# Optimization experiments

Hardware: AMD Instinct MI355X
Metric: run time of the kernel (lower is better)

## Reference

```python
import jax, jax.numpy as jnp
import numpy as np

B, N, DIM = 4, 2048, 1024
HEAD = 16
INTER = 1024
HD = INTER // HEAD  # 64
SCALE = INTER ** (-0.5)


def setup_inputs() -> dict:
    key = jax.random.key(0)
    k1, k2, k3 = jax.random.split(key, 3)
    features = jax.random.normal(k1, (B, N, DIM), dtype=jnp.float32)
    W_qkv = jax.random.normal(k2, (DIM, 3 * INTER), dtype=jnp.float32) * (DIM ** -0.5)
    W_out = jax.random.normal(k3, (INTER, DIM), dtype=jnp.float32) * (INTER ** -0.5)
    return {"features": features, "W_qkv": W_qkv, "W_out": W_out}


def reference(features, W_qkv, W_out):
    # fc_qkv: [b, n, 3*inter], chunk into q, k, v
    qkv = jnp.einsum('bnd,de->bne', features, W_qkv)
    q, k, v = jnp.split(qkv, 3, axis=-1)
    # b n (h d) -> b n h d
    q = q.reshape(B, N, HEAD, HD)
    k = k.reshape(B, N, HEAD, HD)
    v = v.reshape(B, N, HEAD, HD)
    # scores: b h i j  (scale = inter_dim ** -0.5, as in source)
    alpha = jnp.einsum('bihd,bjhd->bhij', q, k) * SCALE
    att = jax.nn.softmax(alpha, axis=-1)
    out = jnp.einsum('bhij,bjhd->bihd', att, v)
    out = out.reshape(B, N, INTER)
    # fc_out (dropout_ratio=0.0 -> identity)
    return jnp.einsum('bni,id->bnd', out, W_out)
```

## Files before the change

### kernel.cpp

```cpp
#include <hip/hip_runtime.h>
#include <stdint.h>

#define BB 4
#define SEQ 2048
#define DMODEL 1024
#define NHEAD 16
#define HDIM 64
#define INTER 1024
#define QSCALE 0.045084220027780106f

#if __has_builtin(__builtin_amdgcn_exp2f)
#define EXP2F(x) __builtin_amdgcn_exp2f(x)
#else
#define EXP2F(x) exp2f(x)
#endif

typedef unsigned short u16;
typedef __attribute__((ext_vector_type(4))) unsigned short u16x4;
typedef __attribute__((ext_vector_type(4))) short s16x4;
typedef __attribute__((ext_vector_type(8))) short s16x8;
typedef __attribute__((ext_vector_type(4))) float f32x4;
typedef __attribute__((ext_vector_type(16))) float f32x16;
typedef __attribute__((ext_vector_type(4))) unsigned int u32x4;

__device__ __forceinline__ u16 f2bf(float f) {
  unsigned int u = __float_as_uint(f);
  u += 0x7FFFu + ((u >> 16) & 1u);
  return (u16)(u >> 16);
}

#if __has_builtin(__builtin_amdgcn_cvt_pk_bf16_f32)
typedef __attribute__((ext_vector_type(2))) __bf16 bf16x2_t;
__device__ __forceinline__ unsigned int pk2bf(float a, float b) {
  bf16x2_t r = __builtin_amdgcn_cvt_pk_bf16_f32(a, b);
  return *reinterpret_cast<unsigned int*>(&r);
}
#else
__device__ __forceinline__ unsigned int pk2bf(float a, float b) {
  return (unsigned int)f2bf(a) | ((unsigned int)f2bf(b) << 16);
}
#endif

__device__ __forceinline__ void async16(const u16* g, u16* l) {
  __builtin_amdgcn_global_load_lds((__attribute__((address_space(1))) void*)(void*)(g),
                                   (__attribute__((address_space(3))) void*)(l),
                                   16, 0, 0);
}

__device__ __forceinline__ void make_pb(const unsigned int* cc, int half,
                                        s16x8& pb0, s16x8& pb1) {
#if __has_builtin(__builtin_amdgcn_permlane32_swap)
  (void)half;
  auto r02 = __builtin_amdgcn_permlane32_swap(cc[0], cc[2], false, false);
  auto r13 = __builtin_amdgcn_permlane32_swap(cc[1], cc[3], false, false);
  auto r46 = __builtin_amdgcn_permlane32_swap(cc[4], cc[6], false, false);
  auto r57 = __builtin_amdgcn_permlane32_swap(cc[5], cc[7], false, false);
  u32x4 w0 = {(unsigned)r02[0], (unsigned)r13[0], (unsigned)r02[1], (unsigned)r13[1]};
  u32x4 w1 = {(unsigned)r46[0], (unsigned)r57[0], (unsigned)r46[1], (unsigned)r57[1]};
#else
  unsigned x0 = __shfl_xor((int)cc[0], 32, 64), x1 = __shfl_xor((int)cc[1], 32, 64);
  unsigned x2 = __shfl_xor((int)cc[2], 32, 64), x3 = __shfl_xor((int)cc[3], 32, 64);
  unsigned x4 = __shfl_xor((int)cc[4], 32, 64), x5 = __shfl_xor((int)cc[5], 32, 64);
  unsigned x6 = __shfl_xor((int)cc[6], 32, 64), x7 = __shfl_xor((int)cc[7], 32, 64);
  u32x4 w0 = {half ? x2 : cc[0], half ? x3 : cc[1],
              half ? cc[2] : x0, half ? cc[3] : x1};
  u32x4 w1 = {half ? x6 : cc[4], half ? x7 : cc[5],
              half ? cc[6] : x4, half ? cc[7] : x5};
#endif
  pb0 = *reinterpret_cast<s16x8*>(&w0);
  pb1 = *reinterpret_cast<s16x8*>(&w1);
}

__global__ __launch_bounds__(256) void prep(
    const float* __restrict__ f, const float* __restrict__ wqkv,
    const float* __restrict__ wout, u16* __restrict__ Xb,
    u16* __restrict__ WqkvT, u16* __restrict__ WoutT) {
  __shared__ float tile[32][33];
  const int bid = blockIdx.x, tid = threadIdx.x;
  if (bid < 8192) {
    int i = (bid * 256 + tid) * 4;
    f32x4 v = *reinterpret_cast<const f32x4*>(f + i);
    uint2 o;
    o.x = pk2bf(v[0], v[1]);
    o.y = pk2bf(v[2], v[3]);
    *reinterpret_cast<uint2*>(Xb + i) = o;
  } else {
    const float* src; u16* dst; int rows, cols, bx, by;
    if (bid < 8192 + 3072) {
      int t = bid - 8192;
      src = wqkv; dst = WqkvT; rows = DMODEL; cols = 3 * INTER;
      bx = t % 96; by = t / 96;
    } else {
      int t = bid - 11264;
      src = wout; dst = WoutT; rows = INTER; cols = DMODEL;
      bx = t & 31; by = t >> 5;
    }
    int c0 = bx * 32, r0 = by * 32, tx = tid & 31, ty = tid >> 5;
    #pragma unroll
    for (int i = ty; i < 32; i += 8) tile[i][tx] = src[(size_t)(r0 + i) * cols + c0 + tx];
    __syncthreads();
    #pragma unroll
    for (int i = ty; i < 32; i += 8)
      dst[(size_t)(c0 + i) * rows + r0 + tx] = f2bf(tile[tx][i]);
  }
}

#define GCOMP(ABUF, BBUF)                                                         \
  {                                                                               \
    s16x8 af[4], bf[4];                                                           \
    _Pragma("unroll")                                                             \
    for (int t = 0; t < 4; t++) {                                                 \
      af[t] = *reinterpret_cast<const s16x8*>(&ABUF[(wr + t * 16 + r) * 32 + q8]); \
      bf[t] = *reinterpret_cast<const s16x8*>(&BBUF[(wc + t * 16 + r) * 32 + q8]); \
    }                                                                             \
    _Pragma("unroll")                                                             \
    for (int i = 0; i < 4; i++)                                                   \
      _Pragma("unroll")                                                           \
      for (int j = 0; j < 4; j++)                                                 \
        acc[i][j] = __builtin_amdgcn_mfma_f32_16x16x32_bf16(af[i], bf[j], acc[i][j], 0, 0, 0); \
  }

template <int MODE>
__global__ __launch_bounds__(256, 2) void gemm_bt(
    const u16* __restrict__ A, const u16* __restrict__ BT,
    float* __restrict__ Cf, u16* __restrict__ Qb, u16* __restrict__ Kp,
    u16* __restrict__ Vp, int K, int ldc) {
  __shared__ u16 As[2][128 * 32];
  __shared__ u16 Bs[2][128 * 32];
  const int tid = threadIdx.x;
  const int wave = tid >> 6, lane = tid & 63;
  const int row0 = blockIdx.y * 128, col0 = blockIdx.x * 128;
  const int wr = (wave >> 1) * 64, wc = (wave & 1) * 64;
  const int r = lane & 15, q8 = (lane >> 4) * 8;

  f32x4 acc[4][4] = {};

  const int sRow = lane >> 2, sK = (lane & 3) * 8;
  const u16* Ag0 = A + (size_t)(row0 + wave * 32 + sRow) * K + sK;
  const u16* Ag1 = Ag0 + (size_t)16 * K;
  const u16* Bg0 = BT + (size_t)(col0 + wave * 32 + sRow) * K + sK;
  const u16* Bg1 = Bg0 + (size_t)16 * K;
  u16* Al0a = &As[0][wave * 1024]; u16* Al1a = Al0a + 512;
  u16* Bl0a = &Bs[0][wave * 1024]; u16* Bl1a = Bl0a + 512;
  u16* Al0b = &As[1][wave * 1024]; u16* Al1b = Al0b + 512;
  u16* Bl0b = &Bs[1][wave * 1024]; u16* Bl1b = Bl0b + 512;

  async16(Ag0, Al0a);
  async16(Ag1, Al1a);
  async16(Bg0, Bl0a);
  async16(Bg1, Bl1a);
  __syncthreads();

  for (int k0 = 0; k0 < K; k0 += 64) {
    if (k0 + 32 < K) {
      async16(Ag0 + k0 + 32, Al0b);
      async16(Ag1 + k0 + 32, Al1b);
      async16(Bg0 + k0 + 32, Bl0b);
      async16(Bg1 + k0 + 32, Bl1b);
    }
    GCOMP(As[0], Bs[0])
    __syncthreads();
    if (k0 + 64 < K) {
      async16(Ag0 + k0 + 64, Al0a);
      async16(Ag1 + k0 + 64, Al1a);
      async16(Bg0 + k0 + 64, Bl0a);
      async16(Bg1 + k0 + 64, Bl1a);
    }
    GCOMP(As[1], Bs[1])
    __syncthreads();
  }

  const int quad = lane >> 4;
  #pragma unroll
  for (int i = 0; i < 4; i++) {
    const int n = row0 + wr + i * 16 + quad * 4;
    const int b = n >> 11, nn = n & (SEQ - 1);
    #pragma unroll
    for (int j = 0; j < 4; j++) {
      const int gc = col0 + wc + j * 16 + r;
      if (MODE == 1) {
        #pragma unroll
        for (int reg = 0; reg < 4; reg++)
          Cf[(size_t)(n + reg) * ldc + gc] = acc[i][j][reg];
      } else if (gc < INTER) {
        size_t base = (size_t)n * INTER + gc;
        #pragma unroll
        for (int reg = 0; reg < 4; reg++)
          Qb[base + (size_t)reg * INTER] = f2bf(acc[i][j][reg] * QSCALE);
      } else if (gc < 2 * INTER) {
        int dim = gc - INTER, h = dim >> 6, d = dim & 63;
        int bh = b * NHEAD + h;
        size_t base = (((size_t)(bh * 64 + (nn >> 5)) * 4 + (d >> 4)) * 64 +
                       ((((d >> 3) & 1) << 5) | (nn & 31))) * 8 + (d & 7);
        #pragma unroll
        for (int reg = 0; reg < 4; reg++)
          Kp[base + reg * 8] = f2bf(acc[i][j][reg]);
      } else {
        int dim = gc - 2 * INTER, h = dim >> 6, d = dim & 63;
        int bh = b * NHEAD + h;
        size_t base = ((((size_t)(bh * 64 + (nn >> 5)) * 2 + ((nn >> 4) & 1)) * 2 +
                        (d >> 5)) * 64 +
                       ((((nn >> 3) & 1) << 5) | (d & 31))) * 8 + (nn & 7);
        uint2 pk;
        pk.x = pk2bf(acc[i][j][0], acc[i][j][1]);
        pk.y = pk2bf(acc[i][j][2], acc[i][j][3]);
        *reinterpret_cast<uint2*>(Vp + base) = pk;
      }
    }
  }
}

#define PSTEP(JCUR, SCUR, SNXT, KNXT, KPF)                                        \
  {                                                                               \
    s16x8 vf[4];                                                                  \
    _Pragma("unroll")                                                             \
    for (int c = 0; c < 4; c++)                                                   \
      vf[c] = *reinterpret_cast<const s16x8*>(vpb + (JCUR) * 2048 + c * 512);     \
    const int jpf = ((JCUR) + 2) & 63;                                            \
    _Pragma("unroll")                                                             \
    for (int c = 0; c < 4; c++)                                                   \
      KPF[c] = *reinterpret_cast<const s16x8*>(kpb + jpf * 2048 + c * 512);       \
    SNXT = (f32x16){};                                                            \
    __builtin_amdgcn_s_setprio(1);                                                \
    _Pragma("unroll")                                                             \
    for (int c = 0; c < 4; c++)                                                   \
      SNXT = __builtin_amdgcn_mfma_f32_32x32x16_bf16(KNXT[c], qf[c], SNXT, 0, 0, 0); \
    __builtin_amdgcn_s_setprio(0);                                                \
    unsigned int cc[8];                                                           \
    _Pragma("unroll")                                                             \
    for (int q = 0; q < 4; q++) {                                                 \
      float p0 = EXP2F(SCUR[q * 4 + 0]), p1 = EXP2F(SCUR[q * 4 + 1]);             \
      float p2 = EXP2F(SCUR[q * 4 + 2]), p3 = EXP2F(SCUR[q * 4 + 3]);             \
      ls += (p0 + p1) + (p2 + p3);                                                \
      cc[q * 2 + 0] = pk2bf(p0, p1);                                              \
      cc[q * 2 + 1] = pk2bf(p2, p3);                                              \
    }                                                                             \
    s16x8 pb0, pb1;                                                               \
    make_pb(cc, half, pb0, pb1);                                                  \
    __builtin_amdgcn_s_setprio(1);                                                \
    ot0 = __builtin_amdgcn_mfma_f32_32x32x16_bf16(vf[0], pb0, ot0, 0, 0, 0);      \
    ot1 = __builtin_amdgcn_mfma_f32_32x32x16_bf16(vf[1], pb0, ot1, 0, 0, 0);      \
    ot0 = __builtin_amdgcn_mfma_f32_32x32x16_bf16(vf[2], pb1, ot0, 0, 0, 0);      \
    ot1 = __builtin_amdgcn_mfma_f32_32x32x16_bf16(vf[3], pb1, ot1, 0, 0, 0);      \
    __builtin_amdgcn_s_setprio(0);                                                \
  }

__global__ __launch_bounds__(64, 3) void attn_kernel(
    const u16* __restrict__ Qb, const u16* __restrict__ Kp,
    const u16* __restrict__ Vp, u16* __restrict__ AO) {
  const int lane = threadIdx.x;
  const int l31 = lane & 31, half = lane >> 5;
  const int bh = blockIdx.x, b = bh >> 4, h = bh & 15;
  const int i0 = blockIdx.y * 32;

  const u16* qbase = Qb + (size_t)(b * SEQ + i0 + l31) * INTER + h * HDIM + half * 8;
  s16x8 qf[4];
  #pragma unroll
  for (int c = 0; c < 4; c++) qf[c] = *reinterpret_cast<const s16x8*>(qbase + c * 16);

  const u16* kpb = Kp + (size_t)bh * (64 * 4 * 512) + lane * 8;
  const u16* vpb = Vp + (size_t)bh * (64 * 4 * 512) + lane * 8;

  f32x16 ot0 = {}, ot1 = {};
  float ls = 0.f;

  s16x8 kX[4], kY[4];
  #pragma unroll
  for (int c = 0; c < 4; c++)
    kX[c] = *reinterpret_cast<const s16x8*>(kpb + 0 * 2048 + c * 512);
  f32x16 stA = {}, stB;
  #pragma unroll
  for (int c = 0; c < 4; c++)
    stA = __builtin_amdgcn_mfma_f32_32x32x16_bf16(kX[c], qf[c], stA, 0, 0, 0);
  #pragma unroll
  for (int c = 0; c < 4; c++)
    kY[c] = *reinterpret_cast<const s16x8*>(kpb + 1 * 2048 + c * 512);

  for (int jb = 0; jb < 64; jb += 2) {
    PSTEP(jb,     stA, stB, kY, kX)
    PSTEP(jb + 1, stB, stA, kX, kY)
  }

  ls += __shfl_xor(ls, 32, 64);
  float rinv = 1.0f / ls;

  u16* orow = AO + (size_t)(b * SEQ + i0 + l31) * INTER + h * HDIM;
  #pragma unroll
  for (int dt = 0; dt < 2; dt++) {
    const f32x16& o = dt ? ot1 : ot0;
    #pragma unroll
    for (int q = 0; q < 4; q++) {
      uint2 pk;
      pk.x = pk2bf(o[q * 4 + 0] * rinv, o[q * 4 + 1] * rinv);
      pk.y = pk2bf(o[q * 4 + 2] * rinv, o[q * 4 + 3] * rinv);
      *reinterpret_cast<uint2*>(orow + dt * 32 + q * 8 + half * 4) = pk;
    }
  }
}

extern "C" void kernel_launch(void* const* d_in, const int* in_sizes, int n_in,
                              void* d_out, int out_size, void* d_ws, size_t ws_size,
                              hipStream_t stream) {
  const float* features = (const float*)d_in[0];
  const float* W_qkv    = (const float*)d_in[1];
  const float* W_out    = (const float*)d_in[2];
  float* out = (float*)d_out;
  char* w = (char*)d_ws;
  u16* Xb    = (u16*)(w);
  u16* WqkvT = (u16*)(w + 16777216);
  u16* WoutT = (u16*)(w + 23068672);
  u16* Qb    = (u16*)(w + 25165824);
  u16* Kp    = (u16*)(w + 41943040);
  u16* Vp    = (u16*)(w + 58720256);
  u16* AO    = (u16*)(w + 75497472);

  prep<<<dim3(12288), dim3(256), 0, stream>>>(features, W_qkv, W_out, Xb, WqkvT, WoutT);
  gemm_bt<0><<<dim3(24, 64), dim3(256), 0, stream>>>(Xb, WqkvT, nullptr, Qb, Kp, Vp,
                                                     DMODEL, 0);
  attn_kernel<<<dim3(64, 64), dim3(64), 0, stream>>>(Qb, Kp, Vp, AO);
  gemm_bt<1><<<dim3(8, 64), dim3(256), 0, stream>>>(AO, WoutT, out, nullptr, nullptr,
                                                    nullptr, INTER, DMODEL);
}
```

Before: 274.7 us.

## Replace QKV projection GEMM with 256x256-tile 8-wave pipelined kernel

Result: slower. 303.0 us (+10.3%).

```diff
diff --git a/kernel.cpp b/kernel.cpp
--- a/kernel.cpp
+++ b/kernel.cpp
@@ -105,84 +105,116 @@
   }
 }
 
-#define GCOMP(ABUF, BBUF)                                                         \
-  {                                                                               \
-    s16x8 af[4], bf[4];                                                           \
-    _Pragma("unroll")                                                             \
-    for (int t = 0; t < 4; t++) {                                                 \
-      af[t] = *reinterpret_cast<const s16x8*>(&ABUF[(wr + t * 16 + r) * 32 + q8]); \
-      bf[t] = *reinterpret_cast<const s16x8*>(&BBUF[(wc + t * 16 + r) * 32 + q8]); \
-    }                                                                             \
-    _Pragma("unroll")                                                             \
-    for (int i = 0; i < 4; i++)                                                   \
-      _Pragma("unroll")                                                           \
-      for (int j = 0; j < 4; j++)                                                 \
-        acc[i][j] = __builtin_amdgcn_mfma_f32_16x16x32_bf16(af[i], bf[j], acc[i][j], 0, 0, 0); \
-  }
-
-template <int MODE>
-__global__ __launch_bounds__(256, 2) void gemm_bt(
+__global__ __launch_bounds__(512, 2) void gemm8p(
     const u16* __restrict__ A, const u16* __restrict__ BT,
-    float* __restrict__ Cf, u16* __restrict__ Qb, u16* __restrict__ Kp,
-    u16* __restrict__ Vp, int K, int ldc) {
-  __shared__ u16 As[2][128 * 32];
-  __shared__ u16 Bs[2][128 * 32];
+    u16* __restrict__ Qb, u16* __restrict__ Kp, u16* __restrict__ Vp) {
+  __shared__ __align__(16) u16 As[2][256 * 64];
+  __shared__ __align__(16) u16 Bs[2][256 * 64];
   const int tid = threadIdx.x;
   const int wave = tid >> 6, lane = tid & 63;
-  const int row0 = blockIdx.y * 128, col0 = blockIdx.x * 128;
-  const int wr = (wave >> 1) * 64, wc = (wave & 1) * 64;
+  const int wm = wave >> 2, wn = wave & 3;
   const int r = lane & 15, q8 = (lane >> 4) * 8;
-
-  f32x4 acc[4][4] = {};
-
-  const int sRow = lane >> 2, sK = (lane & 3) * 8;
-  const u16* Ag0 = A + (size_t)(row0 + wave * 32 + sRow) * K + sK;
-  const u16* Ag1 = Ag0 + (size_t)16 * K;
-  const u16* Bg0 = BT + (size_t)(col0 + wave * 32 + sRow) * K + sK;
-  const u16* Bg1 = Bg0 + (size_t)16 * K;
-  u16* Al0a = &As[0][wave * 1024]; u16* Al1a = Al0a + 512;
-  u16* Bl0a = &Bs[0][wave * 1024]; u16* Bl1a = Bl0a + 512;
-  u16* Al0b = &As[1][wave * 1024]; u16* Al1b = Al0b + 512;
-  u16* Bl0b = &Bs[1][wave * 1024]; u16* Bl1b = Bl0b + 512;
-
-  async16(Ag0, Al0a);
-  async16(Ag1, Al1a);
-  async16(Bg0, Bl0a);
-  async16(Bg1, Bl1a);
-  __syncthreads();
-
-  for (int k0 = 0; k0 < K; k0 += 64) {
-    if (k0 + 32 < K) {
-      async16(Ag0 + k0 + 32, Al0b);
-      async16(Ag1 + k0 + 32, Al1b);
-      async16(Bg0 + k0 + 32, Bl0b);
-      async16(Bg1 + k0 + 32, Bl1b);
-    }
-    GCOMP(As[0], Bs[0])
-    __syncthreads();
-    if (k0 + 64 < K) {
-      async16(Ag0 + k0 + 64, Al0a);
-      async16(Ag1 + k0 + 64, Al1a);
-      async16(Bg0 + k0 + 64, Bl0a);
-      async16(Bg1 + k0 + 64, Bl1a);
-    }
-    GCOMP(As[1], Bs[1])
-    __syncthreads();
+  const int row0 = blockIdx.y * 256, col0 = blockIdx.x * 256;
+
+  const u16* Ag = A + (size_t)(row0 + (tid >> 3)) * 1024 + ((tid & 7) << 3);
+  const u16* Bg = BT + (size_t)(col0 + (tid >> 3)) * 1024 + ((tid & 7) << 3);
+  const int ldsSlot = tid * 8;
+
+  const int aBase = (wm * 128 + r) * 64 + q8;
+  const int bBase = (wn * 64 + r) * 64 + q8;
+
+  f32x4 acc[8][4] = {};
+
+  #pragma unroll
+  for (int i = 0; i < 4; i++) async16(Ag + i * 65536, &As[0][ldsSlot + i * 4096]);
+  #pragma unroll
+  for (int i = 0; i < 4; i++) async16(Bg + i * 65536, &Bs[0][ldsSlot + i * 4096]);
+  asm volatile("s_waitcnt vmcnt(0)" ::: "memory");
+  __builtin_amdgcn_s_barrier();
+
+  for (int kt = 0; kt < 16; kt++) {
+    const int cur = kt & 1;
+    const u16* Ac = &As[0][0] + cur * (256 * 64);
+    const u16* Bc = &Bs[0][0] + cur * (256 * 64);
+    u16* An = &As[0][0] + (1 - cur) * (256 * 64);
+    u16* Bn = &Bs[0][0] + (1 - cur) * (256 * 64);
+    const int kB = (kt + 1) * 64;
+
+    s16x8 af[4], bf[4];
+
+    #pragma unroll
+    for (int nf = 0; nf < 4; nf++)
+      bf[nf] = *reinterpret_cast<const s16x8*>(&Bc[bBase + nf * 1024]);
+    #pragma unroll
+    for (int mf = 0; mf < 4; mf++)
+      af[mf] = *reinterpret_cast<const s16x8*>(&Ac[aBase + mf * 1024]);
+    #pragma unroll
+    for (int i = 0; i < 4; i++) async16(Ag + kB + i * 65536, &An[ldsSlot + i * 4096]);
+    __builtin_amdgcn_s_barrier();
+    __builtin_amdgcn_s_setprio(1);
+    #pragma unroll
+    for (int mf = 0; mf < 4; mf++)
+      #pragma unroll
+      for (int nf = 0; nf < 4; nf++)
+        acc[mf][nf] = __builtin_amdgcn_mfma_f32_16x16x32_bf16(af[mf], bf[nf], acc[mf][nf], 0, 0, 0);
+    __builtin_amdgcn_s_setprio(0);
+    __builtin_amdgcn_s_barrier();
+
+    #pragma unroll
+    for (int mf = 0; mf < 4; mf++)
+      af[mf] = *reinterpret_cast<const s16x8*>(&Ac[aBase + (mf + 4) * 1024]);
+    #pragma unroll
+    for (int i = 0; i < 4; i++) async16(Bg + kB + i * 65536, &Bn[ldsSlot + i * 4096]);
+    __builtin_amdgcn_s_barrier();
+    __builtin_amdgcn_s_setprio(1);
+    #pragma unroll
+    for (int mf = 0; mf < 4; mf++)
+      #pragma unroll
+      for (int nf = 0; nf < 4; nf++)
+        acc[mf + 4][nf] = __builtin_amdgcn_mfma_f32_16x16x32_bf16(af[mf], bf[nf], acc[mf + 4][nf], 0, 0, 0);
+    __builtin_amdgcn_s_setprio(0);
+    __builtin_amdgcn_s_barrier();
+
+    #pragma unroll
+    for (int nf = 0; nf < 4; nf++)
+      bf[nf] = *reinterpret_cast<const s16x8*>(&Bc[bBase + nf * 1024 + 32]);
+    #pragma unroll
+    for (int mf = 0; mf < 4; mf++)
+      af[mf] = *reinterpret_cast<const s16x8*>(&Ac[aBase + mf * 1024 + 32]);
+    __builtin_amdgcn_s_barrier();
+    __builtin_amdgcn_s_setprio(1);
+    #pragma unroll
+    for (int mf = 0; mf < 4; mf++)
+      #pragma unroll
+      for (int nf = 0; nf < 4; nf++)
+        acc[mf][nf] = __builtin_amdgcn_mfma_f32_16x16x32_bf16(af[mf], bf[nf], acc[mf][nf], 0, 0, 0);
+    __builtin_amdgcn_s_setprio(0);
+    __builtin_amdgcn_s_barrier();
+
+    #pragma unroll
+    for (int mf = 0; mf < 4; mf++)
+      af[mf] = *reinterpret_cast<const s16x8*>(&Ac[aBase + (mf + 4) * 1024 + 32]);
+    __builtin_amdgcn_s_barrier();
+    __builtin_amdgcn_s_setprio(1);
+    #pragma unroll
+    for (int mf = 0; mf < 4; mf++)
+      #pragma unroll
+      for (int nf = 0; nf < 4; nf++)
+        acc[mf + 4][nf] = __builtin_amdgcn_mfma_f32_16x16x32_bf16(af[mf], bf[nf], acc[mf + 4][nf], 0, 0, 0);
+    __builtin_amdgcn_s_setprio(0);
+    asm volatile("s_waitcnt vmcnt(0)" ::: "memory");
+    __builtin_amdgcn_s_barrier();
   }
 
   const int quad = lane >> 4;
   #pragma unroll
-  for (int i = 0; i < 4; i++) {
-    const int n = row0 + wr + i * 16 + quad * 4;
+  for (int i = 0; i < 8; i++) {
+    const int n = row0 + wm * 128 + i * 16 + quad * 4;
     const int b = n >> 11, nn = n & (SEQ - 1);
     #pragma unroll
     for (int j = 0; j < 4; j++) {
-      const int gc = col0 + wc + j * 16 + r;
-      if (MODE == 1) {
-        #pragma unroll
-        for (int reg = 0; reg < 4; reg++)
-          Cf[(size_t)(n + reg) * ldc + gc] = acc[i][j][reg];
-      } else if (gc < INTER) {
+      const int gc = col0 + wn * 64 + j * 16 + r;
+      if (gc < INTER) {
         size_t base = (size_t)n * INTER + gc;
         #pragma unroll
         for (int reg = 0; reg < 4; reg++)
@@ -210,6 +242,83 @@
   }
 }
 
+#define GCOMP(ABUF, BBUF)                                                         \
+  {                                                                               \
+    s16x8 af[4], bf[4];                                                           \
+    _Pragma("unroll")                                                             \
+    for (int t = 0; t < 4; t++) {                                                 \
+      af[t] = *reinterpret_cast<const s16x8*>(&ABUF[(wr + t * 16 + r) * 32 + q8]); \
+      bf[t] = *reinterpret_cast<const s16x8*>(&BBUF[(wc + t * 16 + r) * 32 + q8]); \
+    }                                                                             \
+    _Pragma("unroll")                                                             \
+    for (int i = 0; i < 4; i++)                                                   \
+      _Pragma("unroll")                                                           \
+      for (int j = 0; j < 4; j++)                                                 \
+        acc[i][j] = __builtin_amdgcn_mfma_f32_16x16x32_bf16(af[i], bf[j], acc[i][j], 0, 0, 0); \
+  }
+
+__global__ __launch_bounds__(256, 2) void gemm_out(
+    const u16* __restrict__ A, const u16* __restrict__ BT,
+    float* __restrict__ Cf, int K, int ldc) {
+  __shared__ u16 As[2][128 * 32];
+  __shared__ u16 Bs[2][128 * 32];
+  const int tid = threadIdx.x;
+  const int wave = tid >> 6, lane = tid & 63;
+  const int row0 = blockIdx.y * 128, col0 = blockIdx.x * 128;
+  const int wr = (wave >> 1) * 64, wc = (wave & 1) * 64;
+  const int r = lane & 15, q8 = (lane >> 4) * 8;
+
+  f32x4 acc[4][4] = {};
+
+  const int sRow = lane >> 2, sK = (lane & 3) * 8;
+  const u16* Ag0 = A + (size_t)(row0 + wave * 32 + sRow) * K + sK;
+  const u16* Ag1 = Ag0 + (size_t)16 * K;
+  const u16* Bg0 = BT + (size_t)(col0 + wave * 32 + sRow) * K + sK;
+  const u16* Bg1 = Bg0 + (size_t)16 * K;
+  u16* Al0a = &As[0][wave * 1024]; u16* Al1a = Al0a + 512;
+  u16* Bl0a = &Bs[0][wave * 1024]; u16* Bl1a = Bl0a + 512;
+  u16* Al0b = &As[1][wave * 1024]; u16* Al1b = Al0b + 512;
+  u16* Bl0b = &Bs[1][wave * 1024]; u16* Bl1b = Bl0b + 512;
+
+  async16(Ag0, Al0a);
+  async16(Ag1, Al1a);
+  async16(Bg0, Bl0a);
+  async16(Bg1, Bl1a);
+  __syncthreads();
+
+  for (int k0 = 0; k0 < K; k0 += 64) {
+    if (k0 + 32 < K) {
+      async16(Ag0 + k0 + 32, Al0b);
+      async16(Ag1 + k0 + 32, Al1b);
+      async16(Bg0 + k0 + 32, Bl0b);
+      async16(Bg1 + k0 + 32, Bl1b);
+    }
+    GCOMP(As[0], Bs[0])
+    __syncthreads();
+    if (k0 + 64 < K) {
+      async16(Ag0 + k0 + 64, Al0a);
+      async16(Ag1 + k0 + 64, Al1a);
+      async16(Bg0 + k0 + 64, Bl0a);
+      async16(Bg1 + k0 + 64, Bl1a);
+    }
+    GCOMP(As[1], Bs[1])
+    __syncthreads();
+  }
+
+  const int quad = lane >> 4;
+  #pragma unroll
+  for (int i = 0; i < 4; i++) {
+    const int n = row0 + wr + i * 16 + quad * 4;
+    #pragma unroll
+    for (int j = 0; j < 4; j++) {
+      const int gc = col0 + wc + j * 16 + r;
+      #pragma unroll
+      for (int reg = 0; reg < 4; reg++)
+        Cf[(size_t)(n + reg) * ldc + gc] = acc[i][j][reg];
+    }
+  }
+}
+
 #define PSTEP(JCUR, SCUR, SNXT, KNXT, KPF)                                        \
   {                                                                               \
     s16x8 vf[4];                                                                  \
@@ -315,9 +424,7 @@
   u16* AO    = (u16*)(w + 75497472);
 
   prep<<<dim3(12288), dim3(256), 0, stream>>>(features, W_qkv, W_out, Xb, WqkvT, WoutT);
-  gemm_bt<0><<<dim3(24, 64), dim3(256), 0, stream>>>(Xb, WqkvT, nullptr, Qb, Kp, Vp,
-                                                     DMODEL, 0);
+  gemm8p<<<dim3(12, 32), dim3(512), 0, stream>>>(Xb, WqkvT, Qb, Kp, Vp);
   attn_kernel<<<dim3(64, 64), dim3(64), 0, stream>>>(Qb, Kp, Vp, AO);
-  gemm_bt<1><<<dim3(8, 64), dim3(256), 0, stream>>>(AO, WoutT, out, nullptr, nullptr,
-                                                    nullptr, INTER, DMODEL);
-}
+  gemm_out<<<dim3(8, 64), dim3(256), 0, stream>>>(AO, WoutT, out, INTER, DMODEL);
+}
```
